# Kernel tuning notes

Measured on AMD Instinct MI355X. Metric: run time of the kernel, lower is better.

The kernel has to match this reference:

```python
import jax, jax.numpy as jnp
import numpy as np

H = 128            # hardcoded image side in the torch module
TOL = 1e-3         # forward() default tol
MAX_DEPTH = 8      # init kwarg (reduced from 200 for bounded runtime)
LRELU = 0.1        # LeakyReLU negative slope


def _conv(x, w, b, pad):
    # x: [B,Cin,H,H], w: [Cout,Cin,kh,kw]
    y = jax.lax.conv_general_dilated(
        x, w, (1, 1), [(pad, pad), (pad, pad)],
        dimension_numbers=('NCHW', 'OIHW', 'NCHW'))
    if b is not None:
        y = y + b[None, :, None, None]
    return y


def _leaky(x):
    return jnp.where(x >= 0, x, LRELU * x)


def _build_apply_T(d, A, w1, b1, w2, b2, w3, b3, wK, delta, alpha, lambd, beta):
    B = d.shape[0]
    Kc = wK.shape[0]
    dcol = d.reshape(B, -1).T                      # [m, B]
    # ConvTranspose2d(K->1, k=3, pad=1) with weight := convK.weight is the
    # adjoint of convK: regular conv with spatially flipped, channel-swapped kernel.
    wKt = jnp.transpose(jnp.flip(wK, (2, 3)), (1, 0, 2, 3))  # [1,K,3,3]

    def K_op(xk):                                  # [N,B] -> [K*N,B]
        x4 = xk.T.reshape(B, 1, H, H)
        return _conv(x4, wK, None, 1).reshape(B, -1).T

    def Kt_op(pk):                                 # [K*N,B] -> [N,B]
        p4 = pk.T.reshape(B, Kc, H, H)
        return _conv(p4, wKt, None, 1).reshape(B, -1).T

    def R_op(pk):                                  # learned residual denoiser
        p = pk.T.reshape(B, Kc, H, H)
        p = p + _leaky(_conv(p, w1, b1, 2))
        p = p + _leaky(_conv(p, w2, b2, 2))
        p = p + _leaky(_conv(p, w3, b3, 2))
        return p.reshape(B, -1).T

    def ball_proj(w):                              # eval-mode projection
        de = jnp.exp(delta)                        # (1,) -> broadcasts over batch
        dist = jnp.maximum(jnp.linalg.norm(w - dcol, axis=0), 1e-10)
        dn = jnp.linalg.norm(dcol, axis=0)
        scale = jnp.minimum(jnp.ones_like(dist), de * dn / dist)
        return dcol + scale * (w - dcol)

    a = jnp.clip(alpha, 0.0, 2.0)
    bta = jnp.clip(beta, 0.0, 2.0)
    lam = jnp.clip(lambd, 0.0, 2.0)

    def apply_T(x):                                # x: [B,1,H,H]
        xk = x.reshape(B, -1).T                    # [N,B]
        Kxk = K_op(xk)
        # torch: pk = K(xk); pk += lambd*(nuk1 + alpha*(K(xk)-pk)) with nuk1=0
        # and pk==K(xk), so the update is identity -> pk = Kxk.
        pk = R_op(Kxk)
        Axk = A @ xk                               # [m,B]
        # torch: wk = A@xk; temp = wk + lambd*(nuk2 + alpha*(Axk-wk)) = Axk.
        wk = ball_proj(Axk)
        nuk1p = a * (Kxk - pk)
        nuk2p = a * (Axk - wk)
        # nuk1 = nuk2 = 0, so 2*nuk_plus - nuk = 2*nuk_plus
        rk = Kt_op(2.0 * nuk1p) + A.T @ (2.0 * nuk2p)
        xk_new = jnp.clip(xk - bta * rk, 0.0, 1.0)
        return xk_new.T.reshape(B, 1, H, H)

    return apply_T


def setup_inputs() -> dict:
    key = jax.random.key(0)
    ks = jax.random.split(key, 10)
    B, M, N_side, Kc = 8, 4096, 128, 2
    d = jax.random.normal(ks[0], (B, M), jnp.float32)
    A = jax.random.normal(ks[1], (M, N_side * N_side), jnp.float32) / 128.0
    w1 = jax.random.normal(ks[2], (Kc, Kc, 5, 5), jnp.float32) * 0.05
    w2 = jax.random.normal(ks[3], (Kc, Kc, 5, 5), jnp.float32) * 0.05
    w3 = jax.random.normal(ks[4], (Kc, Kc, 5, 5), jnp.float32) * 0.05
    b1 = jnp.zeros((Kc,), jnp.float32)
    b2 = jnp.zeros((Kc,), jnp.float32)
    b3 = jnp.zeros((Kc,), jnp.float32)
    wK = jax.random.normal(ks[5], (Kc, 1, 3, 3), jnp.float32) * 0.1
    return {
        'd': d, 'A': A,
        'w1': w1, 'b1': b1, 'w2': w2, 'b2': b2, 'w3': w3, 'b3': b3,
        'wK': wK,
        'delta': jnp.full((1,), -5.0, jnp.float32),
        'alpha': jnp.full((1,), 0.1, jnp.float32),
        'lambd': jnp.full((1,), 0.1, jnp.float32),
        'beta': jnp.full((1,), 0.1, jnp.float32),
    }


def reference(d, A, w1, b1, w2, b2, w3, b3, wK, delta, alpha, lambd, beta):
    B = d.shape[0]
    apply_T = _build_apply_T(d, A, w1, b1, w2, b2, w3, b3, wK,
                             delta, alpha, lambd, beta)
    x0 = jnp.zeros((B, 1, H, H), d.dtype)
    xp0 = jnp.full((B, 1, H, H), jnp.inf, d.dtype)

    def cond(state):
        x, xp, k = state
        res = jnp.max(jnp.linalg.norm((x - xp).reshape(B, -1), axis=1))
        return (res > TOL) & (k < MAX_DEPTH)

    def body(state):
        x, xp, k = state
        return (apply_T(x), x, k + 1)

    x_star, _, _ = jax.lax.while_loop(cond, body, (x0, xp0, jnp.int32(0)))
    # final differentiable application T(x*)
    return apply_T(x_star)
```

## Files before the change

### kernel.cpp

```cpp
#include <hip/hip_runtime.h>
#include <math.h>

#define HH 128
#define NPIX 16384
#define BB 8
#define MM 4096
#define NN 16384
#define LRELU_S 0.1f

typedef __attribute__((ext_vector_type(8))) short bf16x8;
typedef __attribute__((ext_vector_type(4))) float f32x4;

__device__ __forceinline__ float leaky_(float v){ return v >= 0.f ? v : LRELU_S*v; }
__device__ __forceinline__ float clamp01(float v){ return fminf(fmaxf(v, 0.f), 1.f); }
__device__ __forceinline__ float clamp02(float v){ return fminf(fmaxf(v, 0.f), 2.f); }
__device__ __forceinline__ unsigned short f2bf(float f){
  unsigned u = __float_as_uint(f);
  u = (u + 0x7FFFu + ((u >> 16) & 1u)) >> 16;
  return (unsigned short)u;
}
__device__ __forceinline__ float bf2f(unsigned short s){
  return __uint_as_float(((unsigned)s) << 16);
}

__global__ __launch_bounds__(256) void k_prep(const float* __restrict__ A_,
                                              unsigned short* __restrict__ Abf){
  size_t i = ((size_t)blockIdx.x*256 + threadIdx.x)*8;
  float4 v0 = *(const float4*)&A_[i];
  float4 v1 = *(const float4*)&A_[i+4];
  unsigned short o[8] = { f2bf(v0.x), f2bf(v0.y), f2bf(v0.z), f2bf(v0.w),
                          f2bf(v1.x), f2bf(v1.y), f2bf(v1.z), f2bf(v1.w) };
  *(uint4*)&Abf[i] = *(uint4*)o;
}

__global__ __launch_bounds__(256) void k_prep2(const unsigned short* __restrict__ Abf,
                                               unsigned short* __restrict__ Apk){
  size_t c = (size_t)blockIdx.x*256 + threadIdx.x;
  int col = (int)(c & 15);
  int k8  = (int)((c >> 4) & 2047);
  int mt  = (int)(c >> 15);
  uint4 v = *(const uint4*)&Abf[(size_t)(mt*16 + col)*NN + k8*8];
  *(uint4*)&Apk[c*8] = v;
}

__global__ __launch_bounds__(256) void k_dn(const float* __restrict__ d, float* __restrict__ dn){
  int b = blockIdx.x, t = threadIdx.x;
  float ss = 0.f;
  for (int m=t; m<MM; m+=256){ float v = d[b*MM + m]; ss += v*v; }
  #pragma unroll
  for (int off=32; off; off>>=1) ss += __shfl_down(ss, off);
  __shared__ float red[4];
  if ((t & 63) == 0) red[t>>6] = ss;
  __syncthreads();
  if (t == 0) dn[b] = sqrtf(red[0]+red[1]+red[2]+red[3]);
}

__global__ __launch_bounds__(256) void k_gemm1p(const unsigned short* __restrict__ Apk,
    const unsigned short* __restrict__ xtt, float* __restrict__ e_part){
  __shared__ float part[4][16][16];
  int blk = blockIdx.x;
  int mt = blk >> 2, ng = blk & 3;
  int t = threadIdx.x, w = t >> 6, lane = t & 63;
  int kg = lane >> 4, col = lane & 15;
  const unsigned short* Ap = Apk + (((size_t)mt*2048 + ng*512 + w*128 + kg)*16 + col)*8;
  const unsigned short* Bp = xtt + ((size_t)(ng*512 + w*128 + kg)*16 + col)*8;
  f32x4 acc = {0.f,0.f,0.f,0.f};
  #pragma unroll 8
  for (int s=0; s<32; ++s){
    bf16x8 a = *(const bf16x8*)(Ap + s*512);
    bf16x8 b = *(const bf16x8*)(Bp + s*512);
    acc = __builtin_amdgcn_mfma_f32_16x16x32_bf16(a, b, acc, 0, 0, 0);
  }
  #pragma unroll
  for (int j=0;j<4;++j) part[w][kg*4+j][col] = acc[j];
  __syncthreads();
  int r = t >> 4, b = t & 15;
  float s = part[0][r][b] + part[1][r][b] + part[2][r][b] + part[3][r][b];
  e_part[((size_t)ng*MM + mt*16 + r)*16 + b] = s;
}

__global__ __launch_bounds__(256) void k_phaseB(const unsigned short* __restrict__ Abf,
    const float* __restrict__ e_part, const float* __restrict__ d_,
    const float* __restrict__ x,
    const float* __restrict__ wK, const float* __restrict__ w1, const float* __restrict__ b1,
    const float* __restrict__ w2, const float* __restrict__ b2,
    const float* __restrict__ w3, const float* __restrict__ b3,
    const float* __restrict__ alpha,
    float* __restrict__ up, float* __restrict__ d2p, float* __restrict__ rk1){
  __shared__ float smem[13312];
  __shared__ float wKs[18], w1s[100], w2s[100], w3s[100], bs[6], red8s[64];
  int blk = blockIdx.x, t = threadIdx.x;

  if (blk < 512){
    float (*zs)[128] = (float(*)[128])smem;
    int ms = blk >> 4, nb = blk & 15;
    int m0 = ms*128, n0 = nb*1024;
    for (int i=t; i<1024; i+=256){
      int ml = i >> 3, b = i & 7;
      int m = m0 + ml;
      float s = e_part[(size_t)(0*MM + m)*16 + b]
              + e_part[(size_t)(1*MM + m)*16 + b]
              + e_part[(size_t)(2*MM + m)*16 + b]
              + e_part[(size_t)(3*MM + m)*16 + b];
      zs[b][ml] = s - d_[b*MM + m];
    }
    __syncthreads();
    if (nb == 0){
      if (t < 64){
        int b = t & 7, g = t >> 3;
        float s = 0.f;
        #pragma unroll
        for (int i=0;i<16;++i){ float v = zs[b][g*16+i]; s += v*v; }
        red8s[g*8 + b] = s;
      }
      __syncthreads();
      if (t < 8){
        float s2 = 0.f;
        #pragma unroll
        for (int g=0;g<8;++g) s2 += red8s[g*8 + t];
        d2p[ms*8 + t] = s2;
      }
    }
    int h = t >> 7, cth = t & 127;
    const unsigned short* Ap = Abf + (size_t)(m0 + h*64)*NN + n0 + cth*8;
    float acc[8][8];
    #pragma unroll
    for (int c=0;c<8;++c)
      #pragma unroll
      for (int b=0;b<8;++b) acc[c][b] = 0.f;
    for (int mo=0; mo<64; mo+=8){
      uint4 a8[8];
      #pragma unroll
      for (int u=0;u<8;++u) a8[u] = *(const uint4*)(Ap + (size_t)(mo+u)*NN);
      #pragma unroll
      for (int u=0;u<8;++u){
        float av[8];
        av[0]=bf2f((unsigned short)(a8[u].x & 0xffff)); av[1]=bf2f((unsigned short)(a8[u].x >> 16));
        av[2]=bf2f((unsigned short)(a8[u].y & 0xffff)); av[3]=bf2f((unsigned short)(a8[u].y >> 16));
        av[4]=bf2f((unsigned short)(a8[u].z & 0xffff)); av[5]=bf2f((unsigned short)(a8[u].z >> 16));
        av[6]=bf2f((unsigned short)(a8[u].w & 0xffff)); av[7]=bf2f((unsigned short)(a8[u].w >> 16));
        int ml = h*64 + mo + u;
        #pragma unroll
        for (int b=0;b<8;++b){
          float z = zs[b][ml];
          #pragma unroll
          for (int c=0;c<8;++c) acc[c][b] += av[c]*z;
        }
      }
    }
    int pg = ms*2 + h;
    #pragma unroll
    for (int b=0;b<8;++b){
      float4 v0 = {acc[0][b], acc[1][b], acc[2][b], acc[3][b]};
      float4 v1 = {acc[4][b], acc[5][b], acc[6][b], acc[7][b]};
      float* dst = &up[((size_t)pg*8 + b)*NN + n0 + cth*8];
      *(float4*)dst = v0;
      *(float4*)(dst+4) = v1;
    }
    return;
  }

  int cb = blk - 512;
  int b = cb >> 4, slab = cb & 15, r0 = slab*8;
  float (*xs)[128] = (float(*)[128])&smem[0];
  float (*bufA)[22][128] = (float(*)[22][128])&smem[3072];
  float (*bufB)[18][128] = (float(*)[18][128])&smem[8704];
  float twoa = 2.f*clamp02(alpha[0]);
  for (int i=t;i<18;i+=256) wKs[i]=wK[i];
  for (int i=t;i<100;i+=256){ w1s[i]=w1[i]; w2s[i]=w2[i]; w3s[i]=w3[i]; }
  if (t<2){ bs[t]=b1[t]; bs[2+t]=b2[t]; bs[4+t]=b3[t]; }
  for (int idx=t; idx<24*128; idx+=256){
    int i = idx>>7, j = idx&127, ir = r0-8+i;
    xs[i][j] = ((unsigned)ir < 128u) ? x[b*NPIX + ir*HH + j] : 0.f;
  }
  __syncthreads();
  for (int c=0;c<2;++c)
    for (int idx=t; idx<22*128; idx+=256){
      int i = idx>>7, j = idx&127, ir = r0-7+i;
      float s = 0.f;
      if ((unsigned)ir < 128u){
        #pragma unroll
        for (int di=0;di<3;++di)
          #pragma unroll
          for (int dj=0;dj<3;++dj){
            int jj = j+dj-1;
            if ((unsigned)jj < 128u) s += xs[i+di][jj]*wKs[(c*3+di)*3+dj];
          }
      }
      bufA[c][i][j] = s;
    }
  __syncthreads();
  for (int o=0;o<2;++o)
    for (int idx=t; idx<18*128; idx+=256){
      int i = idx>>7, j = idx&127, ir = r0-5+i;
      float v = 0.f;
      if ((unsigned)ir < 128u){
        float s = bs[o];
        #pragma unroll
        for (int c=0;c<2;++c)
          #pragma unroll
          for (int di=0;di<5;++di)
            #pragma unroll
            for (int dj=0;dj<5;++dj){
              int jj = j+dj-2;
              if ((unsigned)jj < 128u) s += bufA[c][i+di][jj]*w1s[(o*2+c)*25+di*5+dj];
            }
        v = bufA[o][i+2][j] + leaky_(s);
      }
      bufB[o][i][j] = v;
    }
  __syncthreads();
  for (int o=0;o<2;++o)
    for (int idx=t; idx<14*128; idx+=256){
      int i = idx>>7, j = idx&127, ir = r0-3+i;
      float v = 0.f;
      if ((unsigned)ir < 128u){
        float s = bs[2+o];
        #pragma unroll
        for (int c=0;c<2;++c)
          #pragma unroll
          for (int di=0;di<5;++di)
            #pragma unroll
            for (int dj=0;dj<5;++dj){
              int jj = j+dj-2;
              if ((unsigned)jj < 128u) s += bufB[c][i+di][jj]*w2s[(o*2+c)*25+di*5+dj];
            }
        v = bufB[o][i+2][j] + leaky_(s);
      }
      bufA[o][i][j] = v;
    }
  __syncthreads();
  for (int o=0;o<2;++o)
    for (int idx=t; idx<10*128; idx+=256){
      int i = idx>>7, j = idx&127, ir = r0-1+i;
      float v = 0.f;
      if ((unsigned)ir < 128u){
        float s = bs[4+o];
        #pragma unroll
        for (int c=0;c<2;++c)
          #pragma unroll
          for (int di=0;di<5;++di)
            #pragma unroll
            for (int dj=0;dj<5;++dj){
              int jj = j+dj-2;
              if ((unsigned)jj < 128u) s += bufA[c][i+di][jj]*w3s[(o*2+c)*25+di*5+dj];
            }
        v = bufA[o][i+2][j] + leaky_(s);
      }
      bufB[o][i][j] = v;
    }
  __syncthreads();
  for (int c=0;c<2;++c)
    for (int idx=t; idx<10*128; idx+=256){
      int i = idx>>7, j = idx&127, ir = r0-1+i;
      float v = 0.f;
      if ((unsigned)ir < 128u){
        float kx = 0.f;
        #pragma unroll
        for (int di=0;di<3;++di)
          #pragma unroll
          for (int dj=0;dj<3;++dj){
            int jj = j+dj-1;
            if ((unsigned)jj < 128u) kx += xs[i+6+di][jj]*wKs[(c*3+di)*3+dj];
          }
        v = twoa*(kx - bufB[c][i][j]);
      }
      bufA[c][i][j] = v;
    }
  __syncthreads();
  for (int idx=t; idx<8*128; idx+=256){
    int i = idx>>7, j = idx&127, ir = r0+i;
    float s = 0.f;
    #pragma unroll
    for (int c=0;c<2;++c)
      #pragma unroll
      for (int di=0;di<3;++di)
        #pragma unroll
        for (int dj=0;dj<3;++dj){
          int jj = j+dj-1;
          if ((unsigned)jj < 128u) s += bufA[c][i+di][jj]*wKs[(c*3+(2-di))*3+(2-dj)];
        }
    rk1[b*NPIX + ir*HH + j] = s;
  }
}

__global__ __launch_bounds__(256) void k_combine3(const float* __restrict__ up,
    const float* __restrict__ rk1, const float* __restrict__ d2p,
    const float* __restrict__ dn, const float* __restrict__ delta,
    const float* __restrict__ alpha, const float* __restrict__ beta,
    float* __restrict__ x, unsigned short* __restrict__ xtt){
  __shared__ float cf_s[8];
  int t = threadIdx.x;
  if (t < 8){
    float s2 = 0.f;
    #pragma unroll
    for (int ms=0; ms<32; ++ms) s2 += d2p[ms*8 + t];
    float dist = fmaxf(sqrtf(s2), 1e-10f);
    float de = expf(delta[0]);
    float a = clamp02(alpha[0]);
    cf_s[t] = 2.f*a*(1.f - fminf(1.f, de*dn[t]/dist));
  }
  __syncthreads();
  float bta = clamp02(beta[0]);
  int o = blockIdx.x*256 + t;
  int b = o >> 14, pix = o & 16383;
  float s = 0.f;
  #pragma unroll
  for (int p=0; p<64; ++p)
    s += up[((size_t)p*8 + b)*NN + pix];
  float tot = rk1[b*NPIX + pix] + cf_s[b]*s;
  float xn = clamp01(x[b*NPIX + pix] - bta*tot);
  x[b*NPIX + pix] = xn;
  xtt[((size_t)(pix>>3)*16 + b)*8 + (pix&7)] = f2bf(xn);
}

extern "C" void kernel_launch(void* const* d_in, const int* in_sizes, int n_in,
                              void* d_out, int out_size, void* d_ws, size_t ws_size,
                              hipStream_t stream) {
  const float* d_d   = (const float*)d_in[0];
  const float* d_A   = (const float*)d_in[1];
  const float* w1    = (const float*)d_in[2];
  const float* b1    = (const float*)d_in[3];
  const float* w2    = (const float*)d_in[4];
  const float* b2    = (const float*)d_in[5];
  const float* w3    = (const float*)d_in[6];
  const float* b3    = (const float*)d_in[7];
  const float* wK    = (const float*)d_in[8];
  const float* delta = (const float*)d_in[9];
  const float* alpha = (const float*)d_in[10];
  const float* beta  = (const float*)d_in[12];

  char* p = (char*)d_ws;
  unsigned short* Abf = (unsigned short*)p; p += (size_t)MM*NN*2;
  unsigned short* Apk = (unsigned short*)p; p += (size_t)MM*NN*2;
  unsigned short* xtt = (unsigned short*)p; p += (size_t)2048*16*8*2;
  float* x      = (float*)p; p += (size_t)BB*NPIX*4;
  float* rk1    = (float*)p; p += (size_t)BB*NPIX*4;
  float* e_part = (float*)p; p += (size_t)4*MM*16*4;
  float* up     = (float*)p; p += (size_t)64*8*NN*4;
  float* d2p    = (float*)p; p += (size_t)32*8*4;
  float* dnb    = (float*)p; p += 64;

  k_prep<<<MM*NN/(256*8), 256, 0, stream>>>(d_A, Abf);
  k_prep2<<<MM*NN/(256*8), 256, 0, stream>>>(Abf, Apk);
  k_dn<<<BB, 256, 0, stream>>>(d_d, dnb);
  hipMemsetAsync(x, 0, (size_t)BB*NPIX*4, stream);
  hipMemsetAsync(xtt, 0, (size_t)2048*16*8*2, stream);

  for (int it=0; it<9; ++it){
    k_gemm1p<<<1024, 256, 0, stream>>>(Apk, xtt, e_part);
    k_phaseB<<<640, 256, 0, stream>>>(Abf, e_part, d_d, x,
                                      wK, w1, b1, w2, b2, w3, b3, alpha,
                                      up, d2p, rk1);
    k_combine3<<<512, 256, 0, stream>>>(up, rk1, d2p, dnb, delta, alpha, beta, x, xtt);
  }

  hipMemcpyAsync(d_out, x, (size_t)BB*NPIX*4, hipMemcpyDeviceToDevice, stream);
}
```

Measured before the change: 1.469 ms.

## Fuse A bf16 conversion and packing, read packed A in transpose GEMV

Result: slower. 1.877 ms (+27.8%).

```diff
diff --git a/kernel.cpp b/kernel.cpp
--- a/kernel.cpp
+++ b/kernel.cpp
@@ -23,24 +23,27 @@
   return __uint_as_float(((unsigned)s) << 16);
 }
 
-__global__ __launch_bounds__(256) void k_prep(const float* __restrict__ A_,
-                                              unsigned short* __restrict__ Abf){
-  size_t i = ((size_t)blockIdx.x*256 + threadIdx.x)*8;
-  float4 v0 = *(const float4*)&A_[i];
-  float4 v1 = *(const float4*)&A_[i+4];
-  unsigned short o[8] = { f2bf(v0.x), f2bf(v0.y), f2bf(v0.z), f2bf(v0.w),
-                          f2bf(v1.x), f2bf(v1.y), f2bf(v1.z), f2bf(v1.w) };
-  *(uint4*)&Abf[i] = *(uint4*)o;
-}
-
-__global__ __launch_bounds__(256) void k_prep2(const unsigned short* __restrict__ Abf,
-                                               unsigned short* __restrict__ Apk){
-  size_t c = (size_t)blockIdx.x*256 + threadIdx.x;
-  int col = (int)(c & 15);
-  int k8  = (int)((c >> 4) & 2047);
-  int mt  = (int)(c >> 15);
-  uint4 v = *(const uint4*)&Abf[(size_t)(mt*16 + col)*NN + k8*8];
-  *(uint4*)&Apk[c*8] = v;
+__global__ __launch_bounds__(256) void k_prep_pack(const float* __restrict__ A_,
+                                                   unsigned short* __restrict__ Apk){
+  __shared__ unsigned short lb[16][1032];
+  int blk = blockIdx.x;
+  int mt = blk >> 4, ch = blk & 15;
+  int t = threadIdx.x;
+  #pragma unroll
+  for (int i=0;i<16;++i){
+    float4 v = *(const float4*)&A_[(size_t)(mt*16+i)*NN + ch*1024 + t*4];
+    unsigned short o[4] = {f2bf(v.x),f2bf(v.y),f2bf(v.z),f2bf(v.w)};
+    *(uint2*)&lb[i][t*4] = *(uint2*)o;
+  }
+  __syncthreads();
+  size_t base = ((size_t)mt*2048 + ch*128)*128;
+  #pragma unroll
+  for (int j=0;j<8;++j){
+    int o = j*256 + t;
+    int k8l = o >> 4, col = o & 15;
+    uint4 v = *(const uint4*)&lb[col][k8l*8];
+    *(uint4*)&Apk[base + (size_t)o*8] = v;
+  }
 }
 
 __global__ __launch_bounds__(256) void k_dn(const float* __restrict__ d, float* __restrict__ dn){
@@ -79,7 +82,7 @@
   e_part[((size_t)ng*MM + mt*16 + r)*16 + b] = s;
 }
 
-__global__ __launch_bounds__(256) void k_phaseB(const unsigned short* __restrict__ Abf,
+__global__ __launch_bounds__(256) void k_phaseB(const unsigned short* __restrict__ Apk,
     const float* __restrict__ e_part, const float* __restrict__ d_,
     const float* __restrict__ x,
     const float* __restrict__ wK, const float* __restrict__ w1, const float* __restrict__ b1,
@@ -94,7 +97,7 @@
   if (blk < 512){
     float (*zs)[128] = (float(*)[128])smem;
     int ms = blk >> 4, nb = blk & 15;
-    int m0 = ms*128, n0 = nb*1024;
+    int m0 = ms*128, mt0 = ms*8, n0k8 = nb*128;
     for (int i=t; i<1024; i+=256){
       int ml = i >> 3, b = i & 7;
       int m = m0 + ml;
@@ -121,41 +124,48 @@
         d2p[ms*8 + t] = s2;
       }
     }
-    int h = t >> 7, cth = t & 127;
-    const unsigned short* Ap = Abf + (size_t)(m0 + h*64)*NN + n0 + cth*8;
-    float acc[8][8];
-    #pragma unroll
-    for (int c=0;c<8;++c)
-      #pragma unroll
-      for (int b=0;b<8;++b) acc[c][b] = 0.f;
-    for (int mo=0; mo<64; mo+=8){
+    int w = t >> 6;
+    int k8l = (t >> 4) & 3, col = t & 15;
+    for (int k8blk=0; k8blk<8; ++k8blk){
+      int k8g = n0k8 + k8blk*16 + w*4 + k8l;
       uint4 a8[8];
       #pragma unroll
-      for (int u=0;u<8;++u) a8[u] = *(const uint4*)(Ap + (size_t)(mo+u)*NN);
-      #pragma unroll
-      for (int u=0;u<8;++u){
+      for (int mt=0; mt<8; ++mt)
+        a8[mt] = *(const uint4*)&Apk[(((size_t)(mt0+mt)*2048 + k8g)*16 + col)*8];
+      float acc[8][8];
+      #pragma unroll
+      for (int e=0;e<8;++e)
+        #pragma unroll
+        for (int b=0;b<8;++b) acc[e][b] = 0.f;
+      #pragma unroll
+      for (int mt=0; mt<8; ++mt){
         float av[8];
-        av[0]=bf2f((unsigned short)(a8[u].x & 0xffff)); av[1]=bf2f((unsigned short)(a8[u].x >> 16));
-        av[2]=bf2f((unsigned short)(a8[u].y & 0xffff)); av[3]=bf2f((unsigned short)(a8[u].y >> 16));
-        av[4]=bf2f((unsigned short)(a8[u].z & 0xffff)); av[5]=bf2f((unsigned short)(a8[u].z >> 16));
-        av[6]=bf2f((unsigned short)(a8[u].w & 0xffff)); av[7]=bf2f((unsigned short)(a8[u].w >> 16));
-        int ml = h*64 + mo + u;
+        av[0]=bf2f((unsigned short)(a8[mt].x & 0xffff)); av[1]=bf2f((unsigned short)(a8[mt].x >> 16));
+        av[2]=bf2f((unsigned short)(a8[mt].y & 0xffff)); av[3]=bf2f((unsigned short)(a8[mt].y >> 16));
+        av[4]=bf2f((unsigned short)(a8[mt].z & 0xffff)); av[5]=bf2f((unsigned short)(a8[mt].z >> 16));
+        av[6]=bf2f((unsigned short)(a8[mt].w & 0xffff)); av[7]=bf2f((unsigned short)(a8[mt].w >> 16));
+        int ml = mt*16 + col;
         #pragma unroll
         for (int b=0;b<8;++b){
           float z = zs[b][ml];
           #pragma unroll
-          for (int c=0;c<8;++c) acc[c][b] += av[c]*z;
+          for (int e=0;e<8;++e) acc[e][b] += av[e]*z;
         }
       }
-    }
-    int pg = ms*2 + h;
-    #pragma unroll
-    for (int b=0;b<8;++b){
-      float4 v0 = {acc[0][b], acc[1][b], acc[2][b], acc[3][b]};
-      float4 v1 = {acc[4][b], acc[5][b], acc[6][b], acc[7][b]};
-      float* dst = &up[((size_t)pg*8 + b)*NN + n0 + cth*8];
-      *(float4*)dst = v0;
-      *(float4*)(dst+4) = v1;
+      #pragma unroll
+      for (int mask=1; mask<16; mask<<=1)
+        #pragma unroll
+        for (int e=0;e<8;++e)
+          #pragma unroll
+          for (int b=0;b<8;++b) acc[e][b] += __shfl_xor(acc[e][b], mask);
+      if (col < 8){
+        int b = col;
+        float4 v0 = {acc[0][b], acc[1][b], acc[2][b], acc[3][b]};
+        float4 v1 = {acc[4][b], acc[5][b], acc[6][b], acc[7][b]};
+        float* dst = &up[((size_t)ms*8 + b)*NN + k8g*8];
+        *(float4*)dst = v0;
+        *(float4*)(dst+4) = v1;
+      }
     }
     return;
   }
@@ -306,7 +316,7 @@
   int b = o >> 14, pix = o & 16383;
   float s = 0.f;
   #pragma unroll
-  for (int p=0; p<64; ++p)
+  for (int p=0; p<32; ++p)
     s += up[((size_t)p*8 + b)*NN + pix];
   float tot = rk1[b*NPIX + pix] + cf_s[b]*s;
   float xn = clamp01(x[b*NPIX + pix] - bta*tot);
@@ -331,25 +341,23 @@
   const float* beta  = (const float*)d_in[12];
 
   char* p = (char*)d_ws;
-  unsigned short* Abf = (unsigned short*)p; p += (size_t)MM*NN*2;
   unsigned short* Apk = (unsigned short*)p; p += (size_t)MM*NN*2;
   unsigned short* xtt = (unsigned short*)p; p += (size_t)2048*16*8*2;
   float* x      = (float*)p; p += (size_t)BB*NPIX*4;
   float* rk1    = (float*)p; p += (size_t)BB*NPIX*4;
   float* e_part = (float*)p; p += (size_t)4*MM*16*4;
-  float* up     = (float*)p; p += (size_t)64*8*NN*4;
+  float* up     = (float*)p; p += (size_t)32*8*NN*4;
   float* d2p    = (float*)p; p += (size_t)32*8*4;
   float* dnb    = (float*)p; p += 64;
 
-  k_prep<<<MM*NN/(256*8), 256, 0, stream>>>(d_A, Abf);
-  k_prep2<<<MM*NN/(256*8), 256, 0, stream>>>(Abf, Apk);
+  k_prep_pack<<<4096, 256, 0, stream>>>(d_A, Apk);
   k_dn<<<BB, 256, 0, stream>>>(d_d, dnb);
   hipMemsetAsync(x, 0, (size_t)BB*NPIX*4, stream);
   hipMemsetAsync(xtt, 0, (size_t)2048*16*8*2, stream);
 
   for (int it=0; it<9; ++it){
     k_gemm1p<<<1024, 256, 0, stream>>>(Apk, xtt, e_part);
-    k_phaseB<<<640, 256, 0, stream>>>(Abf, e_part, d_d, x,
+    k_phaseB<<<640, 256, 0, stream>>>(Apk, e_part, d_d, x,
                                       wK, w1, b1, w2, b2, w3, b3, alpha,
                                       up, d2p, rk1);
     k_combine3<<<512, 256, 0, stream>>>(up, rk1, d2p, dnb, delta, alpha, beta, x, xtt);
```
